# Optimization experiments

Measured on AMD Instinct MI355X. Metric: run time of the kernel, lower is better.

The kernel has to match this reference:

```python
import jax, jax.numpy as jnp
import numpy as np

N, E = 50000, 800000
IN, HID, OUT, H, REL, RD = 768, 256, 128, 8, 6, 64


def setup_inputs() -> dict:
    key = jax.random.key(0)
    ks = jax.random.split(key, 16)
    g = lambda i, shape, sc: jax.random.normal(ks[i], shape, jnp.float32) * sc
    return dict(
        x=g(0, (N, IN), 1.0),
        edge_index=jax.random.randint(ks[1], (2, E), 0, N),
        edge_type=jax.random.randint(ks[2], (E,), 0, REL),
        rel_emb=g(3, (REL, RD), 0.1),
        W1=g(4, (IN, HID), 0.03),
        att_src1=g(5, (H, HID // H), 0.1),
        att_dst1=g(6, (H, HID // H), 0.1),
        We1=g(7, (RD, HID), 0.1),
        att_e1=g(8, (H, HID // H), 0.1),
        b1=jnp.zeros((HID,), jnp.float32),
        g1=jnp.ones((HID,), jnp.float32),
        beta1=jnp.zeros((HID,), jnp.float32),
        W2=g(9, (HID, OUT), 0.06),
        att_src2=g(10, (1, OUT), 0.1),
        att_dst2=g(11, (1, OUT), 0.1),
        b2=jnp.zeros((OUT,), jnp.float32),
        g2=jnp.ones((OUT,), jnp.float32),
        beta2=jnp.zeros((OUT,), jnp.float32),
    )


def _gat(x, src, dst, W, a_s, a_d, bias, heads, ch, e_feat=None, We=None, a_e=None):
    # PyG GATConv (shared lin, concat=True, negative_slope=0.2, eval-mode dropout)
    n = x.shape[0]
    h = (x @ W).reshape(n, heads, ch)              # [N,H,C]
    al_s = (h * a_s).sum(-1)                       # [N,H]
    al_d = (h * a_d).sum(-1)
    alpha = al_s[src] + al_d[dst]                  # [Etot,H]
    if e_feat is not None:
        e = (e_feat @ We).reshape(-1, heads, ch)
        alpha = alpha + (e * a_e).sum(-1)
    alpha = jax.nn.leaky_relu(alpha, 0.2)
    mx = jax.ops.segment_max(alpha, dst, num_segments=n)   # segment softmax over dst
    ex = jnp.exp(alpha - mx[dst])
    den = jax.ops.segment_sum(ex, dst, num_segments=n)
    w = ex / (den[dst] + 1e-16)
    out = jax.ops.segment_sum(h[src] * w[:, :, None], dst, num_segments=n)
    return out.reshape(n, heads * ch) + bias


def _ln(x, g, b):
    m = x.mean(-1, keepdims=True)
    v = x.var(-1, keepdims=True)
    return (x - m) / jnp.sqrt(v + 1e-5) * g + b


def reference(x, edge_index, edge_type, rel_emb, W1, att_src1, att_dst1, We1, att_e1,
              b1, g1, beta1, W2, att_src2, att_dst2, b2, g2, beta2):
    n = x.shape[0]
    src0, dst0 = edge_index[0], edge_index[1]
    loop = jnp.arange(n)
    src = jnp.concatenate([src0, loop])
    dst = jnp.concatenate([dst0, loop])
    rel_feat = rel_emb[edge_type]                   # [E,RD]
    # self-loop edge_attr = mean of incoming edge_attr (fill_value='mean')
    cnt = jax.ops.segment_sum(jnp.ones((src0.shape[0],), jnp.float32), dst0, num_segments=n)
    self_attr = jax.ops.segment_sum(rel_feat, dst0, num_segments=n) / jnp.maximum(cnt, 1.0)[:, None]
    e_feat = jnp.concatenate([rel_feat, self_attr], 0)
    h = _gat(x, src, dst, W1, att_src1, att_dst1, b1, H, HID // H, e_feat, We1, att_e1)
    h = jax.nn.elu(_ln(h, g1, beta1))
    h = _gat(h, src, dst, W2, att_src2, att_dst2, b2, 1, OUT)
    return _ln(h, g2, beta2)
```

## Files before the change

kernel.cpp:

```cpp
#include <hip/hip_runtime.h>
#include <hip/hip_bf16.h>

#define IN_DIM 768
#define HID 256
#define OUT_DIM 128
#define NHEAD 8
#define NREL 6
#define RD 64

typedef unsigned short ushort_t;
typedef float f32x4 __attribute__((ext_vector_type(4)));
typedef __bf16 bf16x8 __attribute__((ext_vector_type(8)));
typedef unsigned short u16x8 __attribute__((ext_vector_type(8)));
typedef unsigned short u16x4 __attribute__((ext_vector_type(4)));
typedef unsigned short u16x2 __attribute__((ext_vector_type(2)));

typedef const __attribute__((address_space(1))) void* gptr_t;
typedef __attribute__((address_space(3))) void* lptr_t;

static __device__ __forceinline__ float leaky(float x) { return x > 0.f ? x : 0.2f * x; }

static __device__ __forceinline__ ushort_t f2bf(float f) {
    union { __hip_bfloat16 h; ushort_t u; } c;
    c.h = __float2bfloat16(f);
    return c.u;
}

static __device__ __forceinline__ float b2f(ushort_t u) {
    union { unsigned int i; float f; } c;
    c.i = ((unsigned int)u) << 16;
    return c.f;
}

__global__ void count_kernel(const int* __restrict__ dst0, int* __restrict__ deg, int E) {
    int e = blockIdx.x * blockDim.x + threadIdx.x;
    if (e >= E) return;
    atomicAdd(&deg[dst0[e]], 1);
}

__global__ void __launch_bounds__(256) scanA(const int* __restrict__ deg,
                                             int* __restrict__ bsum, int n) {
    __shared__ int sh[4];
    int b = blockIdx.x, t = threadIdx.x;
    int s = 0;
#pragma unroll
    for (int j = 0; j < 4; j++) {
        int idx = b * 1024 + t * 4 + j;
        if (idx < n) s += deg[idx];
    }
    for (int o = 32; o > 0; o >>= 1) s += __shfl_xor(s, o, 64);
    if ((t & 63) == 0) sh[t >> 6] = s;
    __syncthreads();
    if (t == 0) bsum[b] = sh[0] + sh[1] + sh[2] + sh[3];
}

__global__ void __launch_bounds__(256) scanB(const int* __restrict__ bsum,
                                             int* __restrict__ bbase,
                                             int* __restrict__ rowptr, int nb, int n) {
    __shared__ int sh[256];
    int t = threadIdx.x;
    int v = (t < nb) ? bsum[t] : 0;
    sh[t] = v;
    __syncthreads();
    for (int o = 1; o < 256; o <<= 1) {
        int add = (t >= o) ? sh[t - o] : 0;
        __syncthreads();
        sh[t] += add;
        __syncthreads();
    }
    if (t < nb) bbase[t] = sh[t] - v;
    if (t == 255) rowptr[n] = sh[255];
}

__global__ void __launch_bounds__(256) scanC(const int* __restrict__ deg,
                                             const int* __restrict__ bbase,
                                             int* __restrict__ rowptr, int n) {
    __shared__ int sh[256];
    int b = blockIdx.x, t = threadIdx.x;
    int base = b * 1024;
    int loc[4];
    int run = 0;
#pragma unroll
    for (int j = 0; j < 4; j++) {
        int idx = base + t * 4 + j;
        int d = (idx < n) ? deg[idx] : 0;
        loc[j] = run;
        run += d;
    }
    int tot = run;
    sh[t] = run;
    __syncthreads();
    for (int o = 1; o < 256; o <<= 1) {
        int add = (t >= o) ? sh[t - o] : 0;
        __syncthreads();
        sh[t] += add;
        __syncthreads();
    }
    int texcl = sh[t] - tot;
    int bb = bbase[b];
#pragma unroll
    for (int j = 0; j < 4; j++) {
        int idx = base + t * 4 + j;
        if (idx < n) rowptr[idx] = bb + texcl + loc[j];
    }
}

__global__ void scatter_kernel(const int* __restrict__ src0, const int* __restrict__ dst0,
                               const int* __restrict__ ety, const int* __restrict__ rowptr,
                               int* __restrict__ fill, int* __restrict__ src_pk, int E) {
    int e = blockIdx.x * blockDim.x + threadIdx.x;
    if (e >= E) return;
    int d = dst0[e];
    int pos = rowptr[d] + atomicAdd(&fill[d], 1);
    src_pk[pos] = src0[e] | (ety[e] << 24);
}

__global__ void rel_alpha_kernel(const float* __restrict__ rel_emb, const float* __restrict__ We1,
                                 const float* __restrict__ att_e1, float* __restrict__ rel_alpha) {
    int t = threadIdx.x;
    if (t >= NREL * NHEAD) return;
    int r = t / NHEAD, h = t % NHEAD;
    float acc = 0.f;
    for (int c = 0; c < HID / NHEAD; c++) {
        float v = 0.f;
        for (int k = 0; k < RD; k++) v += rel_emb[r * RD + k] * We1[k * HID + h * 32 + c];
        acc += v * att_e1[h * 32 + c];
    }
    rel_alpha[r * NHEAD + h] = acc;
}

__global__ void prep_weights(const float* __restrict__ W1, const float* __restrict__ W2,
                             ushort_t* __restrict__ W1t, ushort_t* __restrict__ W2t) {
    int i = blockIdx.x * 256 + threadIdx.x;
    if (i < IN_DIM * HID) {
        int k = i / HID, n = i % HID;
        W1t[n * IN_DIM + k] = f2bf(W1[i]);
    } else {
        int j = i - IN_DIM * HID;
        if (j < HID * OUT_DIM) {
            int k = j / OUT_DIM, n = j % OUT_DIM;
            W2t[n * HID + k] = f2bf(W2[j]);
        }
    }
}

__global__ void __launch_bounds__(256) conv_bf16(const float* __restrict__ x,
                                                 ushort_t* __restrict__ xb,
                                                 int total, int padtotal) {
    for (long long idx = (long long)(blockIdx.x * 256 + threadIdx.x) * 8; idx < padtotal;
         idx += (long long)gridDim.x * 256 * 8) {
        u16x8 o;
        if (idx < total) {
            float4 f0 = *reinterpret_cast<const float4*>(x + idx);
            float4 f1 = *reinterpret_cast<const float4*>(x + idx + 4);
            o[0] = f2bf(f0.x); o[1] = f2bf(f0.y); o[2] = f2bf(f0.z); o[3] = f2bf(f0.w);
            o[4] = f2bf(f1.x); o[5] = f2bf(f1.y); o[6] = f2bf(f1.z); o[7] = f2bf(f1.w);
        } else {
            o = u16x8{0, 0, 0, 0, 0, 0, 0, 0};
        }
        *reinterpret_cast<u16x8*>(xb + idx) = o;
    }
}

template <int AMODE>
__global__ void __launch_bounds__(256) gemm_lds(const ushort_t* __restrict__ A,
                                                const ushort_t* __restrict__ Bt,
                                                ushort_t* __restrict__ C,
                                                int K, int Nout, int NBlk,
                                                const float* __restrict__ att_s,
                                                const float* __restrict__ att_d,
                                                float* __restrict__ als,
                                                float* __restrict__ ald, int N) {
    __shared__ ushort_t sA[2][128 * 32];
    __shared__ ushort_t sB[2][128 * 32];
    int T = gridDim.x;
    int p = blockIdx.x;
    int q8 = T >> 3, rr8 = T & 7, xc = p & 7, j = p >> 3;
    int l = (xc < rr8 ? xc * (q8 + 1) : rr8 * (q8 + 1) + (xc - rr8) * q8) + j;
    int m0 = (l / NBlk) * 128;
    int n0 = (l % NBlk) * 128;
    int t = threadIdx.x;
    int w = t >> 6, ln = t & 63;
    int wm = (w >> 1) * 64, wn = (w & 1) * 64;

    const ushort_t* ag = A + (size_t)(m0 + w * 32 + (ln >> 2)) * K + (ln & 3) * 8;
    const ushort_t* bg = Bt + (size_t)(n0 + w * 32 + (ln >> 2)) * K + (ln & 3) * 8;

    f32x4 acc[4][4] = {};

    auto stage = [&](int buf, int k0) {
#pragma unroll
        for (int i = 0; i < 2; i++) {
            __builtin_amdgcn_global_load_lds(
                (gptr_t)(const void*)(ag + (size_t)i * 16 * K + k0),
                (lptr_t)(void*)(&sA[buf][(w * 32 + i * 16) * 32]), 16, 0, 0);
            __builtin_amdgcn_global_load_lds(
                (gptr_t)(const void*)(bg + (size_t)i * 16 * K + k0),
                (lptr_t)(void*)(&sB[buf][(w * 32 + i * 16) * 32]), 16, 0, 0);
        }
    };

    int nt = K >> 5;
    stage(0, 0);
    __syncthreads();
    int cur = 0;
    for (int tt = 0; tt < nt; tt++) {
        if (tt + 1 < nt) stage(cur ^ 1, (tt + 1) << 5);
        bf16x8 af[4], bfr[4];
#pragma unroll
        for (int m = 0; m < 4; m++)
            af[m] = *reinterpret_cast<const bf16x8*>(
                &sA[cur][(wm + m * 16 + (ln & 15)) * 32 + (ln >> 4) * 8]);
#pragma unroll
        for (int n = 0; n < 4; n++)
            bfr[n] = *reinterpret_cast<const bf16x8*>(
                &sB[cur][(wn + n * 16 + (ln & 15)) * 32 + (ln >> 4) * 8]);
#pragma unroll
        for (int m = 0; m < 4; m++)
#pragma unroll
            for (int n = 0; n < 4; n++)
                acc[m][n] = __builtin_amdgcn_mfma_f32_16x16x32_bf16(af[m], bfr[n], acc[m][n], 0, 0, 0);
        __syncthreads();
        cur ^= 1;
    }

    int cc = ln & 15, qq = ln >> 4;
#pragma unroll
    for (int m = 0; m < 4; m++) {
#pragma unroll
        for (int rr = 0; rr < 4; rr++) {
            int row = m0 + wm + m * 16 + qq * 4 + rr;
#pragma unroll
            for (int n = 0; n < 4; n++)
                C[(size_t)row * Nout + n0 + wn + n * 16 + cc] = f2bf(acc[m][n][rr]);
        }
    }

    float as_[4], ad_[4];
#pragma unroll
    for (int n = 0; n < 4; n++) {
        int col = n0 + wn + n * 16 + cc;
        as_[n] = att_s[col];
        ad_[n] = att_d[col];
    }

    if constexpr (AMODE == 1) {
        int hbase = (n0 + wn) >> 5;
#pragma unroll
        for (int m = 0; m < 4; m++) {
#pragma unroll
            for (int rr = 0; rr < 4; rr++) {
                int row = m0 + wm + m * 16 + qq * 4 + rr;
                float ps0 = acc[m][0][rr] * as_[0] + acc[m][1][rr] * as_[1];
                float ps1 = acc[m][2][rr] * as_[2] + acc[m][3][rr] * as_[3];
                float pd0 = acc[m][0][rr] * ad_[0] + acc[m][1][rr] * ad_[1];
                float pd1 = acc[m][2][rr] * ad_[2] + acc[m][3][rr] * ad_[3];
#pragma unroll
                for (int o = 1; o < 16; o <<= 1) {
                    ps0 += __shfl_xor(ps0, o, 64);
                    ps1 += __shfl_xor(ps1, o, 64);
                    pd0 += __shfl_xor(pd0, o, 64);
                    pd1 += __shfl_xor(pd1, o, 64);
                }
                if (cc == 0 && row < N) {
                    als[row * NHEAD + hbase] = ps0;
                    als[row * NHEAD + hbase + 1] = ps1;
                    ald[row * NHEAD + hbase] = pd0;
                    ald[row * NHEAD + hbase + 1] = pd1;
                }
            }
        }
    } else {
        __shared__ float sh_s[2][128];
        __shared__ float sh_d[2][128];
#pragma unroll
        for (int m = 0; m < 4; m++) {
#pragma unroll
            for (int rr = 0; rr < 4; rr++) {
                int rib = wm + m * 16 + qq * 4 + rr;
                float ps = acc[m][0][rr] * as_[0] + acc[m][1][rr] * as_[1] +
                           acc[m][2][rr] * as_[2] + acc[m][3][rr] * as_[3];
                float pd = acc[m][0][rr] * ad_[0] + acc[m][1][rr] * ad_[1] +
                           acc[m][2][rr] * ad_[2] + acc[m][3][rr] * ad_[3];
#pragma unroll
                for (int o = 1; o < 16; o <<= 1) {
                    ps += __shfl_xor(ps, o, 64);
                    pd += __shfl_xor(pd, o, 64);
                }
                if (cc == 0) {
                    sh_s[wn >> 6][rib] = ps;
                    sh_d[wn >> 6][rib] = pd;
                }
            }
        }
        __syncthreads();
        if (t < 128) {
            int row = m0 + t;
            if (row < N) {
                als[row] = sh_s[0][t] + sh_s[1][t];
                ald[row] = sh_d[0][t] + sh_d[1][t];
            }
        }
    }
}

__global__ void __launch_bounds__(256) node_agg1(
    const ushort_t* __restrict__ h1b, const float* __restrict__ als, const float* __restrict__ ald,
    const float* __restrict__ rel_alpha, const int* __restrict__ rowptr,
    const int* __restrict__ src_pk,
    const float* __restrict__ b1, const float* __restrict__ g1, const float* __restrict__ beta1,
    ushort_t* __restrict__ out, int N) {
    __shared__ float sh_rel[NREL * NHEAD];
    if (threadIdx.x < NREL * NHEAD) sh_rel[threadIdx.x] = rel_alpha[threadIdx.x];
    __syncthreads();
    int l = threadIdx.x & 63;
    int i = blockIdx.x * 4 + (threadIdx.x >> 6);
    if (i >= N) return;
    int h = l & 7;
    int e8 = l >> 3;
    float als_i = als[i * NHEAD + h];
    float ald_h = ald[i * NHEAD + h];
    float c0, c1, c2, c3;
    {
        u16x4 v = *reinterpret_cast<const u16x4*>(h1b + (size_t)i * HID + 4 * l);
        c0 = b2f(v[0]); c1 = b2f(v[1]); c2 = b2f(v[2]); c3 = b2f(v[3]);
    }
    int base = rowptr[i];
    int deg = rowptr[i + 1] - base;
    const char* hb = reinterpret_cast<const char*>(h1b);
    float acc0 = 0.f, acc1 = 0.f, acc2 = 0.f, acc3 = 0.f;
    float csum = 0.f, rs = 0.f;
    for (int cs = 0; cs < deg; cs += 8) {
        int c = min(8, deg - cs);
        float w = 0.f, ra = 0.f;
        unsigned offv = 0;
        if (e8 < c) {
            int pk = src_pk[base + cs + e8];
            int sv = pk & 0xFFFFFF;
            int tv = (unsigned)pk >> 24;
            ra = sh_rel[tv * NHEAD + h];
            w = __expf(fminf(leaky(als[sv * NHEAD + h] + ald_h + ra), 40.f));
            offv = (unsigned)sv * (HID * 2);
        }
        csum += w;
        rs += ra;
        if (c == 8) {
            float wt[8];
            unsigned of[8];
            u16x4 v[8];
#pragma unroll
            for (int e = 0; e < 8; e++) {
                wt[e] = __shfl(w, e * 8 + e8, 64);
                of[e] = (unsigned)__shfl((int)offv, e * 8, 64);
            }
#pragma unroll
            for (int e = 0; e < 8; e++)
                v[e] = *reinterpret_cast<const u16x4*>(hb + of[e] + 8 * l);
#pragma unroll
            for (int e = 0; e < 8; e++) {
                acc0 += wt[e] * b2f(v[e][0]);
                acc1 += wt[e] * b2f(v[e][1]);
                acc2 += wt[e] * b2f(v[e][2]);
                acc3 += wt[e] * b2f(v[e][3]);
            }
        } else {
            for (int e = 0; e < c; e++) {
                float wt = __shfl(w, e * 8 + e8, 64);
                unsigned of = (unsigned)__shfl((int)offv, e * 8, 64);
                u16x4 v = *reinterpret_cast<const u16x4*>(hb + of + 8 * l);
                acc0 += wt * b2f(v[0]); acc1 += wt * b2f(v[1]);
                acc2 += wt * b2f(v[2]); acc3 += wt * b2f(v[3]);
            }
        }
    }
    for (int o = 8; o < 64; o <<= 1) {
        csum += __shfl_xor(csum, o, 64);
        rs += __shfl_xor(rs, o, 64);
    }
    float selfa = rs / fmaxf((float)deg, 1.0f);
    float wself = __expf(fminf(leaky(als_i + ald_h + selfa), 40.f));
    float stot = csum + wself;
    float s_g = __shfl(stot, e8, 64);
    float w_g = __shfl(wself, e8, 64);
    acc0 += w_g * c0; acc1 += w_g * c1; acc2 += w_g * c2; acc3 += w_g * c3;
    float inv = 1.0f / (s_g + 1e-16f);
    float4 bb = *reinterpret_cast<const float4*>(b1 + 4 * l);
    float y0 = acc0 * inv + bb.x, y1 = acc1 * inv + bb.y;
    float y2 = acc2 * inv + bb.z, y3 = acc3 * inv + bb.w;
    float su = y0 + y1 + y2 + y3;
    float sq = y0 * y0 + y1 * y1 + y2 * y2 + y3 * y3;
    for (int o = 1; o < 64; o <<= 1) {
        su += __shfl_xor(su, o, 64);
        sq += __shfl_xor(sq, o, 64);
    }
    float mean = su * (1.f / 256.f);
    float var = sq * (1.f / 256.f) - mean * mean;
    float rstd = rsqrtf(var + 1e-5f);
    float4 gg = *reinterpret_cast<const float4*>(g1 + 4 * l);
    float4 be = *reinterpret_cast<const float4*>(beta1 + 4 * l);
    float z0 = (y0 - mean) * rstd * gg.x + be.x;
    float z1 = (y1 - mean) * rstd * gg.y + be.y;
    float z2 = (y2 - mean) * rstd * gg.z + be.z;
    float z3 = (y3 - mean) * rstd * gg.w + be.w;
    u16x4 ov;
    ov[0] = f2bf(z0 > 0.f ? z0 : __expf(z0) - 1.f);
    ov[1] = f2bf(z1 > 0.f ? z1 : __expf(z1) - 1.f);
    ov[2] = f2bf(z2 > 0.f ? z2 : __expf(z2) - 1.f);
    ov[3] = f2bf(z3 > 0.f ? z3 : __expf(z3) - 1.f);
    *reinterpret_cast<u16x4*>(out + (size_t)i * HID + 4 * l) = ov;
}

__global__ void __launch_bounds__(256) node_agg2(const ushort_t* __restrict__ h2b,
                                                 const float* __restrict__ als,
                                                 const float* __restrict__ ald,
                                                 const int* __restrict__ rowptr,
                                                 const int* __restrict__ src_pk,
                                                 const float* __restrict__ b2,
                                                 const float* __restrict__ g2,
                                                 const float* __restrict__ beta2,
                                                 float* __restrict__ out, int N) {
    int l = threadIdx.x & 63;
    int i = blockIdx.x * 4 + (threadIdx.x >> 6);
    if (i >= N) return;
    float aldi = ald[i];
    float alsi = als[i];
    float c0, c1;
    {
        u16x2 v = *reinterpret_cast<const u16x2*>(h2b + (size_t)i * OUT_DIM + 2 * l);
        c0 = b2f(v[0]); c1 = b2f(v[1]);
    }
    int base = rowptr[i];
    int deg = rowptr[i + 1] - base;
    const char* hb = reinterpret_cast<const char*>(h2b);
    float acc0 = 0.f, acc1 = 0.f;
    float csum = 0.f;
    for (int cs = 0; cs < deg; cs += 64) {
        int c = min(64, deg - cs);
        float w = 0.f;
        unsigned offv = 0;
        if (l < c) {
            int sv = src_pk[base + cs + l] & 0xFFFFFF;
            w = __expf(fminf(leaky(als[sv] + aldi), 40.f));
            offv = (unsigned)sv * (OUT_DIM * 2);
        }
        csum += w;
        int e = 0;
        for (; e + 8 <= c; e += 8) {
            float wt[8];
            unsigned of[8];
            u16x2 v[8];
#pragma unroll
            for (int jj = 0; jj < 8; jj++) {
                wt[jj] = __shfl(w, e + jj, 64);
                of[jj] = (unsigned)__shfl((int)offv, e + jj, 64);
            }
#pragma unroll
            for (int jj = 0; jj < 8; jj++)
                v[jj] = *reinterpret_cast<const u16x2*>(hb + of[jj] + 4 * l);
#pragma unroll
            for (int jj = 0; jj < 8; jj++) {
                acc0 += wt[jj] * b2f(v[jj][0]);
                acc1 += wt[jj] * b2f(v[jj][1]);
            }
        }
        for (; e < c; e++) {
            float wt = __shfl(w, e, 64);
            unsigned of = (unsigned)__shfl((int)offv, e, 64);
            u16x2 v = *reinterpret_cast<const u16x2*>(hb + of + 4 * l);
            acc0 += wt * b2f(v[0]); acc1 += wt * b2f(v[1]);
        }
    }
    for (int o = 1; o < 64; o <<= 1) csum += __shfl_xor(csum, o, 64);
    float wself = __expf(fminf(leaky(alsi + aldi), 40.f));
    float s = csum + wself;
    acc0 += wself * c0; acc1 += wself * c1;
    float inv = 1.0f / (s + 1e-16f);
    float2 bb = *reinterpret_cast<const float2*>(b2 + 2 * l);
    float y0 = acc0 * inv + bb.x, y1 = acc1 * inv + bb.y;
    float su = y0 + y1, sq = y0 * y0 + y1 * y1;
    for (int o = 1; o < 64; o <<= 1) {
        su += __shfl_xor(su, o, 64);
        sq += __shfl_xor(sq, o, 64);
    }
    float mean = su * (1.f / 128.f);
    float var = sq * (1.f / 128.f) - mean * mean;
    float rstd = rsqrtf(var + 1e-5f);
    float2 gg = *reinterpret_cast<const float2*>(g2 + 2 * l);
    float2 be = *reinterpret_cast<const float2*>(beta2 + 2 * l);
    float2 ov;
    ov.x = (y0 - mean) * rstd * gg.x + be.x;
    ov.y = (y1 - mean) * rstd * gg.y + be.y;
    *reinterpret_cast<float2*>(out + (size_t)i * OUT_DIM + 2 * l) = ov;
}

extern "C" void kernel_launch(void* const* d_in, const int* in_sizes, int n_in,
                              void* d_out, int out_size, void* d_ws, size_t ws_size,
                              hipStream_t stream) {
    const float* x = (const float*)d_in[0];
    const int* ei = (const int*)d_in[1];
    const int* ety = (const int*)d_in[2];
    const float* rel_emb = (const float*)d_in[3];
    const float* W1 = (const float*)d_in[4];
    const float* att_s1 = (const float*)d_in[5];
    const float* att_d1 = (const float*)d_in[6];
    const float* We1 = (const float*)d_in[7];
    const float* att_e1 = (const float*)d_in[8];
    const float* b1 = (const float*)d_in[9];
    const float* g1 = (const float*)d_in[10];
    const float* beta1 = (const float*)d_in[11];
    const float* W2 = (const float*)d_in[12];
    const float* att_s2 = (const float*)d_in[13];
    const float* att_d2 = (const float*)d_in[14];
    const float* b2 = (const float*)d_in[15];
    const float* g2 = (const float*)d_in[16];
    const float* beta2 = (const float*)d_in[17];

    int N = in_sizes[0] / IN_DIM;
    int E = in_sizes[1] / 2;
    int Mpad = ((N + 127) / 128) * 128;
    const int* src0 = ei;
    const int* dst0 = ei + E;

    char* ws = (char*)d_ws;
    size_t off = 0;
    auto alloc = [&](size_t bytes) -> void* {
        off = (off + 255) & ~(size_t)255;
        void* p = ws + off;
        off += bytes;
        return p;
    };
    int* deg = (int*)alloc((size_t)N * 4);
    int* fill = (int*)alloc((size_t)N * 4);
    int* rowptr = (int*)alloc((size_t)(N + 1) * 4);
    int* src_pk = (int*)alloc((size_t)E * 4);
    int nb = (N + 1023) >> 10;
    int* bsum = (int*)alloc((size_t)nb * 4);
    int* bbase = (int*)alloc((size_t)nb * 4);
    float* rel_alpha = (float*)alloc(NREL * NHEAD * 4);
    float* als1 = (float*)alloc((size_t)N * NHEAD * 4);
    float* ald1 = (float*)alloc((size_t)N * NHEAD * 4);
    float* al2s = (float*)alloc((size_t)N * 4);
    float* al2d = (float*)alloc((size_t)N * 4);
    ushort_t* W1t = (ushort_t*)alloc((size_t)HID * IN_DIM * 2);
    ushort_t* W2t = (ushort_t*)alloc((size_t)OUT_DIM * HID * 2);
    ushort_t* h1b = (ushort_t*)alloc((size_t)Mpad * HID * 2);
    ushort_t* xb = (ushort_t*)alloc((size_t)Mpad * IN_DIM * 2);
    ushort_t* h1pb = xb;
    ushort_t* h2b = h1b;

    hipMemsetAsync(deg, 0, (size_t)N * 4, stream);
    hipMemsetAsync(fill, 0, (size_t)N * 4, stream);

    int eb = (E + 255) / 256;
    count_kernel<<<eb, 256, 0, stream>>>(dst0, deg, E);
    scanA<<<nb, 256, 0, stream>>>(deg, bsum, N);
    scanB<<<1, 256, 0, stream>>>(bsum, bbase, rowptr, nb, N);
    scanC<<<nb, 256, 0, stream>>>(deg, bbase, rowptr, N);
    scatter_kernel<<<eb, 256, 0, stream>>>(src0, dst0, ety, rowptr, fill, src_pk, E);
    rel_alpha_kernel<<<1, 64, 0, stream>>>(rel_emb, We1, att_e1, rel_alpha);
    prep_weights<<<(IN_DIM * HID + HID * OUT_DIM + 255) / 256, 256, 0, stream>>>(W1, W2, W1t, W2t);
    conv_bf16<<<2048, 256, 0, stream>>>(x, xb, N * IN_DIM, Mpad * IN_DIM);

    int NB1 = HID / 128;
    int T1 = (Mpad / 128) * NB1;
    gemm_lds<1><<<T1, 256, 0, stream>>>(xb, W1t, h1b, IN_DIM, HID, NB1,
                                        att_s1, att_d1, als1, ald1, N);
    hipMemsetAsync(h1pb + (size_t)N * HID, 0, (size_t)(Mpad - N) * HID * 2, stream);
    node_agg1<<<(N + 3) / 4, 256, 0, stream>>>(h1b, als1, ald1, rel_alpha, rowptr, src_pk,
                                               b1, g1, beta1, h1pb, N);

    int NB2 = OUT_DIM / 128;
    int T2 = (Mpad / 128) * NB2;
    gemm_lds<2><<<T2, 256, 0, stream>>>(h1pb, W2t, h2b, HID, OUT_DIM, NB2,
                                        att_s2, att_d2, al2s, al2d, N);
    node_agg2<<<(N + 3) / 4, 256, 0, stream>>>(h2b, al2s, al2d, rowptr, src_pk, b2, g2, beta2,
                                               (float*)d_out, N);
}
```

Baseline: 375.8 us.

## Fuse fp32-to-bf16 input conversion into the first GEMM's LDS load path

Removes the separate conv_bf16 pass over x. The first GEMM now loads fp32 x tiles into swizzled LDS with global_load_lds and converts them to bf16 while building MFMA fragments. This avoids writing and re-reading a bf16 copy of the 50000x768 input. In exchange, the GEMM reads twice the bytes per tile, drops double buffering (a single LDS stage with two barriers per k-step), and converts each A element redundantly across the two N-blocks.

New measurement: 345.3 us. -8.1%, faster.

```diff
diff --git a/kernel.cpp b/kernel.cpp
--- a/kernel.cpp
+++ b/kernel.cpp
@@ -144,33 +144,144 @@
     }
 }
 
-__global__ void __launch_bounds__(256) conv_bf16(const float* __restrict__ x,
-                                                 ushort_t* __restrict__ xb,
-                                                 int total, int padtotal) {
-    for (long long idx = (long long)(blockIdx.x * 256 + threadIdx.x) * 8; idx < padtotal;
-         idx += (long long)gridDim.x * 256 * 8) {
-        u16x8 o;
-        if (idx < total) {
-            float4 f0 = *reinterpret_cast<const float4*>(x + idx);
-            float4 f1 = *reinterpret_cast<const float4*>(x + idx + 4);
-            o[0] = f2bf(f0.x); o[1] = f2bf(f0.y); o[2] = f2bf(f0.z); o[3] = f2bf(f0.w);
-            o[4] = f2bf(f1.x); o[5] = f2bf(f1.y); o[6] = f2bf(f1.z); o[7] = f2bf(f1.w);
-        } else {
-            o = u16x8{0, 0, 0, 0, 0, 0, 0, 0};
-        }
-        *reinterpret_cast<u16x8*>(xb + idx) = o;
-    }
-}
-
-template <int AMODE>
-__global__ void __launch_bounds__(256) gemm_lds(const ushort_t* __restrict__ A,
-                                                const ushort_t* __restrict__ Bt,
-                                                ushort_t* __restrict__ C,
-                                                int K, int Nout, int NBlk,
-                                                const float* __restrict__ att_s,
-                                                const float* __restrict__ att_d,
-                                                float* __restrict__ als,
-                                                float* __restrict__ ald, int N) {
+__global__ void __launch_bounds__(256) gemm_f32a(const float* __restrict__ Af,
+                                                 const ushort_t* __restrict__ Bt,
+                                                 ushort_t* __restrict__ C,
+                                                 int K, int Nout, int NBlk,
+                                                 const float* __restrict__ att_s,
+                                                 const float* __restrict__ att_d,
+                                                 float* __restrict__ als,
+                                                 float* __restrict__ ald, int N) {
+    __shared__ float sAf[128 * 64];
+    __shared__ ushort_t sB[128 * 64];
+    int T = gridDim.x;
+    int p = blockIdx.x;
+    int q8 = T >> 3, rr8 = T & 7, xc = p & 7, jj0 = p >> 3;
+    int l = (xc < rr8 ? xc * (q8 + 1) : rr8 * (q8 + 1) + (xc - rr8) * q8) + jj0;
+    int m0 = (l / NBlk) * 128;
+    int n0 = (l % NBlk) * 128;
+    int t = threadIdx.x;
+    int w = t >> 6, ln = t & 63;
+    int wm = (w >> 1) * 64, wn = (w & 1) * 64;
+
+    const float* agp[8];
+#pragma unroll
+    for (int i = 0; i < 8; i++) {
+        int rl = w * 32 + i * 4 + (ln >> 4);
+        int rg = min(m0 + rl, N - 1);
+        int cc = (ln & 15) ^ (rl & 15);
+        agp[i] = Af + (size_t)rg * K + (cc << 2);
+    }
+    const ushort_t* bgp[4];
+#pragma unroll
+    for (int i = 0; i < 4; i++) {
+        int rl = w * 32 + i * 8 + (ln >> 3);
+        int cc = (ln & 7) ^ (ln >> 3);
+        bgp[i] = Bt + (size_t)(n0 + rl) * K + (cc << 3);
+    }
+
+    f32x4 acc[4][4] = {};
+
+    for (int k0 = 0; k0 < K; k0 += 64) {
+#pragma unroll
+        for (int i = 0; i < 8; i++)
+            __builtin_amdgcn_global_load_lds((gptr_t)(const void*)(agp[i] + k0),
+                                             (lptr_t)(void*)(&sAf[(w * 32 + i * 4) * 64]),
+                                             16, 0, 0);
+#pragma unroll
+        for (int i = 0; i < 4; i++)
+            __builtin_amdgcn_global_load_lds((gptr_t)(const void*)(bgp[i] + k0),
+                                             (lptr_t)(void*)(&sB[(w * 32 + i * 8) * 64]),
+                                             16, 0, 0);
+        __syncthreads();
+#pragma unroll
+        for (int ks = 0; ks < 2; ks++) {
+            bf16x8 af[4], bfr[4];
+#pragma unroll
+            for (int m = 0; m < 4; m++) {
+                int r = wm + m * 16 + (ln & 15);
+                int key = ln & 15;
+                int c0 = ks * 8 + (ln >> 4) * 2;
+                const f32x4* rowp = reinterpret_cast<const f32x4*>(&sAf[r * 64]);
+                f32x4 lo = rowp[c0 ^ key];
+                f32x4 hi = rowp[(c0 + 1) ^ key];
+                union { u16x8 u; bf16x8 b; } cv;
+                cv.u[0] = f2bf(lo[0]); cv.u[1] = f2bf(lo[1]);
+                cv.u[2] = f2bf(lo[2]); cv.u[3] = f2bf(lo[3]);
+                cv.u[4] = f2bf(hi[0]); cv.u[5] = f2bf(hi[1]);
+                cv.u[6] = f2bf(hi[2]); cv.u[7] = f2bf(hi[3]);
+                af[m] = cv.b;
+            }
+#pragma unroll
+            for (int n = 0; n < 4; n++) {
+                int r = wn + n * 16 + (ln & 15);
+                int key = ln & 7;
+                int cB = ks * 4 + (ln >> 4);
+                bfr[n] = *reinterpret_cast<const bf16x8*>(&sB[r * 64 + ((cB ^ key) << 3)]);
+            }
+#pragma unroll
+            for (int m = 0; m < 4; m++)
+#pragma unroll
+                for (int n = 0; n < 4; n++)
+                    acc[m][n] = __builtin_amdgcn_mfma_f32_16x16x32_bf16(af[m], bfr[n], acc[m][n], 0, 0, 0);
+        }
+        __syncthreads();
+    }
+
+    int cc = ln & 15, qq = ln >> 4;
+#pragma unroll
+    for (int m = 0; m < 4; m++) {
+#pragma unroll
+        for (int rr = 0; rr < 4; rr++) {
+            int row = m0 + wm + m * 16 + qq * 4 + rr;
+#pragma unroll
+            for (int n = 0; n < 4; n++)
+                C[(size_t)row * Nout + n0 + wn + n * 16 + cc] = f2bf(acc[m][n][rr]);
+        }
+    }
+
+    float as_[4], ad_[4];
+#pragma unroll
+    for (int n = 0; n < 4; n++) {
+        int col = n0 + wn + n * 16 + cc;
+        as_[n] = att_s[col];
+        ad_[n] = att_d[col];
+    }
+    int hbase = (n0 + wn) >> 5;
+#pragma unroll
+    for (int m = 0; m < 4; m++) {
+#pragma unroll
+        for (int rr = 0; rr < 4; rr++) {
+            int row = m0 + wm + m * 16 + qq * 4 + rr;
+            float ps0 = acc[m][0][rr] * as_[0] + acc[m][1][rr] * as_[1];
+            float ps1 = acc[m][2][rr] * as_[2] + acc[m][3][rr] * as_[3];
+            float pd0 = acc[m][0][rr] * ad_[0] + acc[m][1][rr] * ad_[1];
+            float pd1 = acc[m][2][rr] * ad_[2] + acc[m][3][rr] * ad_[3];
+#pragma unroll
+            for (int o = 1; o < 16; o <<= 1) {
+                ps0 += __shfl_xor(ps0, o, 64);
+                ps1 += __shfl_xor(ps1, o, 64);
+                pd0 += __shfl_xor(pd0, o, 64);
+                pd1 += __shfl_xor(pd1, o, 64);
+            }
+            if (cc == 0 && row < N) {
+                als[row * NHEAD + hbase] = ps0;
+                als[row * NHEAD + hbase + 1] = ps1;
+                ald[row * NHEAD + hbase] = pd0;
+                ald[row * NHEAD + hbase + 1] = pd1;
+            }
+        }
+    }
+}
+
+__global__ void __launch_bounds__(256) gemm_lds2(const ushort_t* __restrict__ A,
+                                                 const ushort_t* __restrict__ Bt,
+                                                 ushort_t* __restrict__ C,
+                                                 int K, int Nout, int NBlk,
+                                                 const float* __restrict__ att_s,
+                                                 const float* __restrict__ att_d,
+                                                 float* __restrict__ als,
+                                                 float* __restrict__ ald, int N) {
     __shared__ ushort_t sA[2][128 * 32];
     __shared__ ushort_t sB[2][128 * 32];
     int T = gridDim.x;
@@ -243,63 +354,34 @@
         as_[n] = att_s[col];
         ad_[n] = att_d[col];
     }
-
-    if constexpr (AMODE == 1) {
-        int hbase = (n0 + wn) >> 5;
-#pragma unroll
-        for (int m = 0; m < 4; m++) {
-#pragma unroll
-            for (int rr = 0; rr < 4; rr++) {
-                int row = m0 + wm + m * 16 + qq * 4 + rr;
-                float ps0 = acc[m][0][rr] * as_[0] + acc[m][1][rr] * as_[1];
-                float ps1 = acc[m][2][rr] * as_[2] + acc[m][3][rr] * as_[3];
-                float pd0 = acc[m][0][rr] * ad_[0] + acc[m][1][rr] * ad_[1];
-                float pd1 = acc[m][2][rr] * ad_[2] + acc[m][3][rr] * ad_[3];
-#pragma unroll
-                for (int o = 1; o < 16; o <<= 1) {
-                    ps0 += __shfl_xor(ps0, o, 64);
-                    ps1 += __shfl_xor(ps1, o, 64);
-                    pd0 += __shfl_xor(pd0, o, 64);
-                    pd1 += __shfl_xor(pd1, o, 64);
-                }
-                if (cc == 0 && row < N) {
-                    als[row * NHEAD + hbase] = ps0;
-                    als[row * NHEAD + hbase + 1] = ps1;
-                    ald[row * NHEAD + hbase] = pd0;
-                    ald[row * NHEAD + hbase + 1] = pd1;
-                }
-            }
-        }
-    } else {
-        __shared__ float sh_s[2][128];
-        __shared__ float sh_d[2][128];
-#pragma unroll
-        for (int m = 0; m < 4; m++) {
-#pragma unroll
-            for (int rr = 0; rr < 4; rr++) {
-                int rib = wm + m * 16 + qq * 4 + rr;
-                float ps = acc[m][0][rr] * as_[0] + acc[m][1][rr] * as_[1] +
-                           acc[m][2][rr] * as_[2] + acc[m][3][rr] * as_[3];
-                float pd = acc[m][0][rr] * ad_[0] + acc[m][1][rr] * ad_[1] +
-                           acc[m][2][rr] * ad_[2] + acc[m][3][rr] * ad_[3];
-#pragma unroll
-                for (int o = 1; o < 16; o <<= 1) {
-                    ps += __shfl_xor(ps, o, 64);
-                    pd += __shfl_xor(pd, o, 64);
-                }
-                if (cc == 0) {
-                    sh_s[wn >> 6][rib] = ps;
-                    sh_d[wn >> 6][rib] = pd;
-                }
-            }
-        }
-        __syncthreads();
-        if (t < 128) {
-            int row = m0 + t;
-            if (row < N) {
-                als[row] = sh_s[0][t] + sh_s[1][t];
-                ald[row] = sh_d[0][t] + sh_d[1][t];
-            }
+    __shared__ float sh_s[2][128];
+    __shared__ float sh_d[2][128];
+#pragma unroll
+    for (int m = 0; m < 4; m++) {
+#pragma unroll
+        for (int rr = 0; rr < 4; rr++) {
+            int rib = wm + m * 16 + qq * 4 + rr;
+            float ps = acc[m][0][rr] * as_[0] + acc[m][1][rr] * as_[1] +
+                       acc[m][2][rr] * as_[2] + acc[m][3][rr] * as_[3];
+            float pd = acc[m][0][rr] * ad_[0] + acc[m][1][rr] * ad_[1] +
+                       acc[m][2][rr] * ad_[2] + acc[m][3][rr] * ad_[3];
+#pragma unroll
+            for (int o = 1; o < 16; o <<= 1) {
+                ps += __shfl_xor(ps, o, 64);
+                pd += __shfl_xor(pd, o, 64);
+            }
+            if (cc == 0) {
+                sh_s[wn >> 6][rib] = ps;
+                sh_d[wn >> 6][rib] = pd;
+            }
+        }
+    }
+    __syncthreads();
+    if (t < 128) {
+        int row = m0 + t;
+        if (row < N) {
+            als[row] = sh_s[0][t] + sh_s[1][t];
+            ald[row] = sh_d[0][t] + sh_d[1][t];
         }
     }
 }
@@ -544,8 +626,7 @@
     ushort_t* W1t = (ushort_t*)alloc((size_t)HID * IN_DIM * 2);
     ushort_t* W2t = (ushort_t*)alloc((size_t)OUT_DIM * HID * 2);
     ushort_t* h1b = (ushort_t*)alloc((size_t)Mpad * HID * 2);
-    ushort_t* xb = (ushort_t*)alloc((size_t)Mpad * IN_DIM * 2);
-    ushort_t* h1pb = xb;
+    ushort_t* h1pb = (ushort_t*)alloc((size_t)Mpad * HID * 2);
     ushort_t* h2b = h1b;
 
     hipMemsetAsync(deg, 0, (size_t)N * 4, stream);
@@ -559,20 +640,19 @@
     scatter_kernel<<<eb, 256, 0, stream>>>(src0, dst0, ety, rowptr, fill, src_pk, E);
     rel_alpha_kernel<<<1, 64, 0, stream>>>(rel_emb, We1, att_e1, rel_alpha);
     prep_weights<<<(IN_DIM * HID + HID * OUT_DIM + 255) / 256, 256, 0, stream>>>(W1, W2, W1t, W2t);
-    conv_bf16<<<2048, 256, 0, stream>>>(x, xb, N * IN_DIM, Mpad * IN_DIM);
 
     int NB1 = HID / 128;
     int T1 = (Mpad / 128) * NB1;
-    gemm_lds<1><<<T1, 256, 0, stream>>>(xb, W1t, h1b, IN_DIM, HID, NB1,
-                                        att_s1, att_d1, als1, ald1, N);
+    gemm_f32a<<<T1, 256, 0, stream>>>(x, W1t, h1b, IN_DIM, HID, NB1,
+                                      att_s1, att_d1, als1, ald1, N);
     hipMemsetAsync(h1pb + (size_t)N * HID, 0, (size_t)(Mpad - N) * HID * 2, stream);
     node_agg1<<<(N + 3) / 4, 256, 0, stream>>>(h1b, als1, ald1, rel_alpha, rowptr, src_pk,
                                                b1, g1, beta1, h1pb, N);
 
     int NB2 = OUT_DIM / 128;
     int T2 = (Mpad / 128) * NB2;
-    gemm_lds<2><<<T2, 256, 0, stream>>>(h1pb, W2t, h2b, HID, OUT_DIM, NB2,
-                                        att_s2, att_d2, al2s, al2d, N);
+    gemm_lds2<<<T2, 256, 0, stream>>>(h1pb, W2t, h2b, HID, OUT_DIM, NB2,
+                                      att_s2, att_d2, al2s, al2d, N);
     node_agg2<<<(N + 3) / 4, 256, 0, stream>>>(h2b, al2s, al2d, rowptr, src_pk, b2, g2, beta2,
                                                (float*)d_out, N);
 }
```
